# Kernel optimization log

Measured on AMD Instinct MI355X. Metric: run time of the kernel, lower is better.

The kernel has to match this reference:

```python
import jax, jax.numpy as jnp
import numpy as np

DIM = 768
HEADS = 12
HEAD_DIM = DIM // HEADS
ROPE_BASE = 100.0  # Dust3R uses freq=100 for its rotary embedding


def apply_rope(x):
    # x: [B, H, N, D] -> rotary embedding over token index (rotate-half form)
    B, H, N, D = x.shape
    pos = jnp.arange(N, dtype=jnp.float32)
    inv_freq = 1.0 / (ROPE_BASE ** (jnp.arange(0, D, 2, dtype=jnp.float32) / D))
    ang = pos[:, None] * inv_freq[None, :]            # [N, D/2]
    cos = jnp.concatenate([jnp.cos(ang), jnp.cos(ang)], axis=-1).astype(x.dtype)  # [N, D]
    sin = jnp.concatenate([jnp.sin(ang), jnp.sin(ang)], axis=-1).astype(x.dtype)
    x1, x2 = jnp.split(x, 2, axis=-1)
    x_rot = jnp.concatenate([-x2, x1], axis=-1)
    return x * cos + x_rot * sin


def setup_inputs() -> dict:
    key = jax.random.key(0)
    ks = jax.random.split(key, 8)
    B, N = 8, 1024
    scale = 0.02
    return {
        "query": jax.random.normal(ks[0], (B, N, DIM), jnp.float32),
        "key": jax.random.normal(ks[1], (B, N, DIM), jnp.float32),
        "value": jax.random.normal(ks[2], (B, N, DIM), jnp.float32),
        "Wq": jax.random.normal(ks[3], (DIM, DIM), jnp.float32) * scale,
        "Wk": jax.random.normal(ks[4], (DIM, DIM), jnp.float32) * scale,
        "Wv": jax.random.normal(ks[5], (DIM, DIM), jnp.float32) * scale,
        "Wo": jax.random.normal(ks[6], (DIM, DIM), jnp.float32) * scale,
        "bo": jax.random.normal(ks[7], (DIM,), jnp.float32) * scale,
    }


def reference(query, key, value, Wq, Wk, Wv, Wo, bo):
    B, Nq, C = query.shape
    H, D = HEADS, HEAD_DIM
    sm_scale = D ** -0.5
    # Linear projections (torch Linear: x @ W.T), split heads -> [B, H, N, D]
    q = jnp.einsum('bnc,dc->bnd', query, Wq).reshape(B, Nq, H, D).transpose(0, 2, 1, 3)
    k = jnp.einsum('bnc,dc->bnd', key, Wk).reshape(B, -1, H, D).transpose(0, 2, 1, 3)
    v = jnp.einsum('bnc,dc->bnd', value, Wv).reshape(B, -1, H, D).transpose(0, 2, 1, 3)
    q = apply_rope(q)
    k = apply_rope(k)
    attn = jnp.einsum('bhqd,bhkd->bhqk', q, k) * sm_scale
    attn = jax.nn.softmax(attn, axis=-1)
    x = jnp.einsum('bhqk,bhkd->bhqd', attn, v)
    x = x.transpose(0, 2, 1, 3).reshape(B, Nq, C)
    return jnp.einsum('bnc,dc->bnd', x, Wo) + bo
```

## Files before the change

### kernel.cpp

```cpp
#include <hip/hip_runtime.h>
#include <cmath>

typedef __bf16 bf16x8 __attribute__((ext_vector_type(8)));
typedef float f32x4 __attribute__((ext_vector_type(4)));
typedef unsigned short u16;

#define MFMA_BF16 __builtin_amdgcn_mfma_f32_16x16x32_bf16

__device__ __forceinline__ u16 f2bf(float f) {
  unsigned int u = __float_as_uint(f);
  u = (u + 0x7fffu + ((u >> 16) & 1u)) >> 16;
  return (u16)u;
}

__device__ __forceinline__ void async16(const u16* g, u16* l) {
  __builtin_amdgcn_global_load_lds(
      (__attribute__((address_space(1))) void*)g,
      (__attribute__((address_space(3))) void*)l, 16, 0, 0);
}

__global__ __launch_bounds__(256) void cvt_bf16(const float4* __restrict__ in,
                                                uint2* __restrict__ out, int n4) {
  int i = blockIdx.x * 256 + threadIdx.x;
  if (i >= n4) return;
  float4 f = in[i];
  uint2 o;
  o.x = (unsigned)f2bf(f.x) | ((unsigned)f2bf(f.y) << 16);
  o.y = (unsigned)f2bf(f.z) | ((unsigned)f2bf(f.w) << 16);
  out[i] = o;
}

__global__ __launch_bounds__(256) void cvt_all(
    const float4* s0, const float4* s1, const float4* s2, const float4* s3,
    const float4* s4, const float4* s5, const float4* s6,
    uint2* d0, uint2* d1, uint2* d2, uint2* d3, uint2* d4, uint2* d5, uint2* d6) {
  int i = blockIdx.x * 256 + threadIdx.x;
  const float4* src;
  uint2* dst;
  int off;
  if (i < 1572864)      { src = s0; dst = d0; off = i; }
  else if (i < 3145728) { src = s1; dst = d1; off = i - 1572864; }
  else if (i < 4718592) { src = s2; dst = d2; off = i - 3145728; }
  else {
    int j = i - 4718592;
    int w = j / 147456;
    off = j - w * 147456;
    src = (w == 0) ? s3 : (w == 1) ? s4 : (w == 2) ? s5 : s6;
    dst = (w == 0) ? d3 : (w == 1) ? d4 : (w == 2) ? d5 : d6;
  }
  float4 f = src[off];
  uint2 o;
  o.x = (unsigned)f2bf(f.x) | ((unsigned)f2bf(f.y) << 16);
  o.y = (unsigned)f2bf(f.z) | ((unsigned)f2bf(f.w) << 16);
  dst[off] = o;
}

__device__ __forceinline__ void gemm_body(const u16* __restrict__ Ag,
                                          const u16* __restrict__ Wg,
                                          void* __restrict__ OutP,
                                          const float* __restrict__ bias,
                                          int mode, int bx, int by) {
  __shared__ u16 As[128][64];
  __shared__ u16 Bs[64][64];
  const int tid  = threadIdx.x;
  const int lane = tid & 63, wv = tid >> 6;
  const int l15  = lane & 15, quad = lane >> 4;
  const int row0 = bx * 128, col0 = by * 64;
  const int wm = wv * 32;
  const int swA = l15 & 7;

  f32x4 acc[2][4];
#pragma unroll
  for (int i = 0; i < 2; ++i)
#pragma unroll
    for (int j = 0; j < 4; ++j) acc[i][j] = (f32x4){0.f, 0.f, 0.f, 0.f};

  for (int kb0 = 0; kb0 < 768; kb0 += 64) {
#pragma unroll
    for (int rr = 0; rr < 4; ++rr) {
      int c = rr * 256 + tid;
      int row = c >> 3, cp = c & 7;
      int gc = cp ^ (row & 7);
      async16(&Ag[(size_t)(row0 + row) * 768 + kb0 + gc * 8], &As[row][cp * 8]);
    }
#pragma unroll
    for (int rr = 0; rr < 2; ++rr) {
      int c = rr * 256 + tid;
      int row = c >> 3, cp = c & 7;
      int gc = cp ^ (row & 7);
      async16(&Wg[(size_t)(col0 + row) * 768 + kb0 + gc * 8], &Bs[row][cp * 8]);
    }
    __syncthreads();
#pragma unroll
    for (int kd = 0; kd < 2; ++kd) {
      int cpk = (((kd * 4 + quad) ^ swA)) * 8;
      bf16x8 af[2], bfr[4];
      af[0] = *(const bf16x8*)&As[wm + l15][cpk];
      af[1] = *(const bf16x8*)&As[wm + 16 + l15][cpk];
#pragma unroll
      for (int nt = 0; nt < 4; ++nt) bfr[nt] = *(const bf16x8*)&Bs[nt * 16 + l15][cpk];
#pragma unroll
      for (int mt = 0; mt < 2; ++mt)
#pragma unroll
        for (int nt = 0; nt < 4; ++nt)
          acc[mt][nt] = MFMA_BF16(af[mt], bfr[nt], acc[mt][nt], 0, 0, 0);
    }
    __syncthreads();
  }

  if (mode == 3) {
    float* O = (float*)OutP;
#pragma unroll
    for (int mt = 0; mt < 2; ++mt)
#pragma unroll
      for (int r = 0; r < 4; ++r) {
        int m = row0 + wm + mt * 16 + quad * 4 + r;
#pragma unroll
        for (int nt = 0; nt < 4; ++nt) {
          int c = col0 + nt * 16 + l15;
          O[(size_t)m * 768 + c] = acc[mt][nt][r] + bias[c];
        }
      }
  } else if (mode == 2) {
    u16* O = (u16*)OutP;
#pragma unroll
    for (int mt = 0; mt < 2; ++mt)
#pragma unroll
      for (int r = 0; r < 4; ++r) {
        int m = row0 + wm + mt * 16 + quad * 4 + r;
        int b = m >> 10, n = m & 1023;
#pragma unroll
        for (int nt = 0; nt < 4; ++nt) {
          int c = col0 + nt * 16 + l15;
          O[(size_t)(b * 768 + c) * 1024 + n] = f2bf(acc[mt][nt][r]);
        }
      }
  } else {
    u16* O = (u16*)OutP;
    const float scale = (mode == 0) ? 0.125f * 1.44269504088896f : 1.0f;
    const float invf0 = exp2f(-6.6438561897747395f * (float)l15 * (1.0f / 32.0f));
    const float invf1 = exp2f(-6.6438561897747395f * (float)(16 + l15) * (1.0f / 32.0f));
#pragma unroll
    for (int mt = 0; mt < 2; ++mt)
#pragma unroll
      for (int r = 0; r < 4; ++r) {
        int m = row0 + wm + mt * 16 + quad * 4 + r;
        int b = m >> 10, n = m & 1023;
        float fn = (float)n;
        size_t rowbase = (size_t)b * 786432 + (size_t)n * 64;
#pragma unroll
        for (int nt = 0; nt < 2; ++nt) {
          float sv, cv;
          __sincosf(fn * (nt ? invf1 : invf0), &sv, &cv);
          float x1 = acc[mt][nt][r], x2 = acc[mt][nt + 2][r];
          int c1 = col0 + nt * 16 + l15;
          int c2 = c1 + 32;
          O[rowbase + (size_t)(c1 >> 6) * 65536 + (c1 & 63)] = f2bf((x1 * cv - x2 * sv) * scale);
          O[rowbase + (size_t)(c2 >> 6) * 65536 + (c2 & 63)] = f2bf((x2 * cv + x1 * sv) * scale);
        }
      }
  }
}

__global__ __launch_bounds__(256, 3) void gemm768(const u16* __restrict__ A,
                                                  const u16* __restrict__ W,
                                                  void* __restrict__ OutP,
                                                  const float* __restrict__ bias,
                                                  int mode) {
  gemm_body(A, W, OutP, bias, mode, blockIdx.x, blockIdx.y);
}

__global__ __launch_bounds__(256, 3) void gemm_qkv(
    const u16* __restrict__ xq, const u16* __restrict__ xk, const u16* __restrict__ xv,
    const u16* __restrict__ wq, const u16* __restrict__ wk, const u16* __restrict__ wv,
    u16* __restrict__ qb, u16* __restrict__ kb, u16* __restrict__ vtb) {
  int z = blockIdx.z;
  const u16* A = (z == 0) ? xq : (z == 1) ? xk : xv;
  const u16* W = (z == 0) ? wq : (z == 1) ? wk : wv;
  void* O      = (z == 0) ? (void*)qb : (z == 1) ? (void*)kb : (void*)vtb;
  gemm_body(A, W, O, nullptr, z, blockIdx.x, blockIdx.y);
}

__global__ __launch_bounds__(256, 2) void attn_fused(const u16* __restrict__ Q,
                                                     const u16* __restrict__ K,
                                                     const u16* __restrict__ Vt,
                                                     u16* __restrict__ X) {
  __shared__ u16 KsF[2 * 64 * 32];
  __shared__ u16 VsF[2 * 64 * 32];
  __shared__ u16 Ps[128 * 88];

  const int tid  = threadIdx.x;
  const int lane = tid & 63, wv = tid >> 6;
  const int l15  = lane & 15, quad = lane >> 4;
  const int bh = blockIdx.x, qt = blockIdx.y;
  const size_t base = (size_t)bh * 65536;
  const int sw8 = (quad ^ ((l15 >> 1) & 3)) * 8;

  const u16* Qg = Q + base + (size_t)qt * 8192;
#pragma unroll
  for (int rr = 0; rr < 4; ++rr) {
    int c = rr * 256 + tid;
    async16(&Qg[c * 8], &Ps[c * 8]);
  }
  __syncthreads();
  bf16x8 qf[2][2];
#pragma unroll
  for (int mt = 0; mt < 2; ++mt)
#pragma unroll
    for (int kd = 0; kd < 2; ++kd)
      qf[mt][kd] = *(const bf16x8*)&Ps[(wv * 32 + mt * 16 + l15) * 64 + kd * 32 + quad * 8];
  __syncthreads();

  f32x4 o[2][4];
  float lsum[2][4];
#pragma unroll
  for (int mt = 0; mt < 2; ++mt) {
#pragma unroll
    for (int nt = 0; nt < 4; ++nt) o[mt][nt] = (f32x4){0.f, 0.f, 0.f, 0.f};
#pragma unroll
    for (int r = 0; r < 4; ++r) lsum[mt][r] = 0.f;
  }

  const u16* Kb = K + base;
  const u16* Vb = Vt + base;

  for (int kt = 0; kt < 1024; kt += 64) {
#pragma unroll
    for (int rr = 0; rr < 2; ++rr) {
      int c = rr * 256 + tid;
      int sub = c >> 8, rowi = (c >> 2) & 63, colc = c & 3;
      int cs = (colc ^ ((rowi >> 1) & 3)) * 8;
      async16(&Kb[(size_t)(kt + rowi) * 64 + sub * 32 + cs], &KsF[c * 8]);
      async16(&Vb[(size_t)rowi * 1024 + kt + sub * 32 + cs], &VsF[c * 8]);
    }
    __syncthreads();

    f32x4 s[2][4];
#pragma unroll
    for (int ct = 0; ct < 4; ++ct) {
      bf16x8 kf0 = *(const bf16x8*)&KsF[(ct * 16 + l15) * 32 + sw8];
      bf16x8 kf1 = *(const bf16x8*)&KsF[2048 + (ct * 16 + l15) * 32 + sw8];
#pragma unroll
      for (int mt = 0; mt < 2; ++mt) {
        f32x4 t = (f32x4){0.f, 0.f, 0.f, 0.f};
        t = MFMA_BF16(qf[mt][0], kf0, t, 0, 0, 0);
        t = MFMA_BF16(qf[mt][1], kf1, t, 0, 0, 0);
        s[mt][ct] = t;
      }
    }

#pragma unroll
    for (int mt = 0; mt < 2; ++mt)
#pragma unroll
      for (int ct = 0; ct < 4; ++ct)
#pragma unroll
        for (int r = 0; r < 4; ++r) {
          float p = __builtin_amdgcn_exp2f(s[mt][ct][r]);
          lsum[mt][r] += p;
          unsigned u = __float_as_uint(p);
          Ps[(wv * 32 + mt * 16 + quad * 4 + r) * 88 + ct * 16 + l15] =
              (u16)((u + 0x8000u) >> 16);
        }

#pragma unroll
    for (int ks = 0; ks < 2; ++ks) {
      bf16x8 pf0 = *(const bf16x8*)&Ps[(wv * 32 + l15) * 88 + ks * 32 + quad * 8];
      bf16x8 pf1 = *(const bf16x8*)&Ps[(wv * 32 + 16 + l15) * 88 + ks * 32 + quad * 8];
#pragma unroll
      for (int nt = 0; nt < 4; ++nt) {
        bf16x8 vf = *(const bf16x8*)&VsF[ks * 2048 + (nt * 16 + l15) * 32 + sw8];
        o[0][nt] = MFMA_BF16(pf0, vf, o[0][nt], 0, 0, 0);
        o[1][nt] = MFMA_BF16(pf1, vf, o[1][nt], 0, 0, 0);
      }
    }
    __syncthreads();
  }

  const int b = bh / 12, h = bh % 12;
#pragma unroll
  for (int mt = 0; mt < 2; ++mt)
#pragma unroll
    for (int r = 0; r < 4; ++r) {
      float l = lsum[mt][r];
#pragma unroll
      for (int d = 1; d < 16; d <<= 1) l += __shfl_xor(l, d, 16);
      float inv = __builtin_amdgcn_rcpf(l);
      int n = qt * 128 + wv * 32 + mt * 16 + quad * 4 + r;
      size_t rowoff = ((size_t)(b * 1024 + n)) * 768 + h * 64;
#pragma unroll
      for (int nt = 0; nt < 4; ++nt)
        X[rowoff + nt * 16 + l15] = f2bf(o[mt][nt][r] * inv);
    }
}

extern "C" void kernel_launch(void* const* d_in, const int* in_sizes, int n_in,
                              void* d_out, int out_size, void* d_ws, size_t ws_size,
                              hipStream_t stream) {
  const float* qin = (const float*)d_in[0];
  const float* kin = (const float*)d_in[1];
  const float* vin = (const float*)d_in[2];
  const float* Wq  = (const float*)d_in[3];
  const float* Wk  = (const float*)d_in[4];
  const float* Wv  = (const float*)d_in[5];
  const float* Wo  = (const float*)d_in[6];
  const float* bo  = (const float*)d_in[7];
  char* ws = (char*)d_ws;

  if (ws_size >= 80216064) {
    u16* xq16 = (u16*)(ws + 0);
    u16* xk16 = (u16*)(ws + 12582912);
    u16* xv16 = (u16*)(ws + 25165824);
    u16* qb   = (u16*)(ws + 37748736);
    u16* kb   = (u16*)(ws + 50331648);
    u16* vtb  = (u16*)(ws + 62914560);
    u16* wq16 = (u16*)(ws + 75497472);
    u16* wk16 = wq16 + 589824;
    u16* wv16 = wk16 + 589824;
    u16* wo16 = wv16 + 589824;
    u16* X    = xq16;

    cvt_all<<<20736, 256, 0, stream>>>(
        (const float4*)qin, (const float4*)kin, (const float4*)vin,
        (const float4*)Wq, (const float4*)Wk, (const float4*)Wv, (const float4*)Wo,
        (uint2*)xq16, (uint2*)xk16, (uint2*)xv16,
        (uint2*)wq16, (uint2*)wk16, (uint2*)wv16, (uint2*)wo16);
    gemm_qkv<<<dim3(64, 12, 3), 256, 0, stream>>>(xq16, xk16, xv16, wq16, wk16, wv16,
                                                  qb, kb, vtb);
    attn_fused<<<dim3(96, 8), 256, 0, stream>>>(qb, kb, vtb, X);
    gemm768<<<dim3(64, 12), 256, 0, stream>>>(X, wo16, d_out, bo, 3);
  } else {
    u16* xbuf = (u16*)(ws + 0);
    u16* qb   = (u16*)(ws + 12582912);
    u16* kb   = (u16*)(ws + 25165824);
    u16* vtb  = (u16*)(ws + 37748736);
    u16* wq16 = (u16*)(ws + 50331648);
    u16* wk16 = wq16 + 589824;
    u16* wv16 = wk16 + 589824;
    u16* wo16 = wv16 + 589824;

    cvt_bf16<<<576, 256, 0, stream>>>((const float4*)Wq, (uint2*)wq16, 147456);
    cvt_bf16<<<576, 256, 0, stream>>>((const float4*)Wk, (uint2*)wk16, 147456);
    cvt_bf16<<<576, 256, 0, stream>>>((const float4*)Wv, (uint2*)wv16, 147456);
    cvt_bf16<<<576, 256, 0, stream>>>((const float4*)Wo, (uint2*)wo16, 147456);

    dim3 ggrid(64, 12);
    cvt_bf16<<<6144, 256, 0, stream>>>((const float4*)qin, (uint2*)xbuf, 1572864);
    gemm768<<<ggrid, 256, 0, stream>>>(xbuf, wq16, (void*)qb, nullptr, 0);
    cvt_bf16<<<6144, 256, 0, stream>>>((const float4*)kin, (uint2*)xbuf, 1572864);
    gemm768<<<ggrid, 256, 0, stream>>>(xbuf, wk16, (void*)kb, nullptr, 1);
    cvt_bf16<<<6144, 256, 0, stream>>>((const float4*)vin, (uint2*)xbuf, 1572864);
    gemm768<<<ggrid, 256, 0, stream>>>(xbuf, wv16, (void*)vtb, nullptr, 2);

    attn_fused<<<dim3(96, 8), 256, 0, stream>>>(qb, kb, vtb, xbuf);

    gemm768<<<ggrid, 256, 0, stream>>>(xbuf, wo16, d_out, bo, 3);
  }
}
```

Baseline: 214.5 us.

## Widen QKV GEMM tiles to 128x128 and process 128 keys per attention stage

The QKV projection now uses a dedicated kernel with 128x128 output tiles, where each wave computes a 64x64 sub-tile. This raises operand reuse per LDS load and halves the number of blocks. The attention kernel loads 128 keys/values per barrier and processes them as two 64-key halves, halving the number of syncs. It also shrinks the P buffer padding and raises its occupancy hint to 3, and the output GEMM's hint goes to 4. The changes trade more registers and LDS per block for fewer barriers and fewer global reloads, at the risk of spilling or lower occupancy.

After: 235.3 us. +9.7%, slower.

```diff
diff --git a/kernel.cpp b/kernel.cpp
--- a/kernel.cpp
+++ b/kernel.cpp
@@ -55,6 +55,65 @@
   dst[off] = o;
 }
 
+template <int MT>
+__device__ __forceinline__ void gemm_epilogue(f32x4 (&acc)[MT][4], void* OutP,
+                                              const float* bias, int mode,
+                                              int row0, int colbase, int wm,
+                                              int l15, int quad) {
+  if (mode == 3) {
+    float* O = (float*)OutP;
+#pragma unroll
+    for (int mt = 0; mt < MT; ++mt)
+#pragma unroll
+      for (int r = 0; r < 4; ++r) {
+        int m = row0 + wm + mt * 16 + quad * 4 + r;
+#pragma unroll
+        for (int nt = 0; nt < 4; ++nt) {
+          int c = colbase + nt * 16 + l15;
+          O[(size_t)m * 768 + c] = acc[mt][nt][r] + bias[c];
+        }
+      }
+  } else if (mode == 2) {
+    u16* O = (u16*)OutP;
+#pragma unroll
+    for (int mt = 0; mt < MT; ++mt)
+#pragma unroll
+      for (int r = 0; r < 4; ++r) {
+        int m = row0 + wm + mt * 16 + quad * 4 + r;
+        int b = m >> 10, n = m & 1023;
+#pragma unroll
+        for (int nt = 0; nt < 4; ++nt) {
+          int c = colbase + nt * 16 + l15;
+          O[(size_t)(b * 768 + c) * 1024 + n] = f2bf(acc[mt][nt][r]);
+        }
+      }
+  } else {
+    u16* O = (u16*)OutP;
+    const float scale = (mode == 0) ? 0.125f * 1.44269504088896f : 1.0f;
+    const float invf0 = exp2f(-6.6438561897747395f * (float)l15 * (1.0f / 32.0f));
+    const float invf1 = exp2f(-6.6438561897747395f * (float)(16 + l15) * (1.0f / 32.0f));
+#pragma unroll
+    for (int mt = 0; mt < MT; ++mt)
+#pragma unroll
+      for (int r = 0; r < 4; ++r) {
+        int m = row0 + wm + mt * 16 + quad * 4 + r;
+        int b = m >> 10, n = m & 1023;
+        float fn = (float)n;
+        size_t rowbase = (size_t)b * 786432 + (size_t)n * 64;
+#pragma unroll
+        for (int nt = 0; nt < 2; ++nt) {
+          float sv, cv;
+          __sincosf(fn * (nt ? invf1 : invf0), &sv, &cv);
+          float x1 = acc[mt][nt][r], x2 = acc[mt][nt + 2][r];
+          int c1 = colbase + nt * 16 + l15;
+          int c2 = c1 + 32;
+          O[rowbase + (size_t)(c1 >> 6) * 65536 + (c1 & 63)] = f2bf((x1 * cv - x2 * sv) * scale);
+          O[rowbase + (size_t)(c2 >> 6) * 65536 + (c2 & 63)] = f2bf((x2 * cv + x1 * sv) * scale);
+        }
+      }
+  }
+}
+
 __device__ __forceinline__ void gemm_body(const u16* __restrict__ Ag,
                                           const u16* __restrict__ Wg,
                                           void* __restrict__ OutP,
@@ -63,10 +122,10 @@
   __shared__ u16 As[128][64];
   __shared__ u16 Bs[64][64];
   const int tid  = threadIdx.x;
-  const int lane = tid & 63, wv = tid >> 6;
+  const int lane = tid & 63, wvid = tid >> 6;
   const int l15  = lane & 15, quad = lane >> 4;
   const int row0 = bx * 128, col0 = by * 64;
-  const int wm = wv * 32;
+  const int wm = wvid * 32;
   const int swA = l15 & 7;
 
   f32x4 acc[2][4];
@@ -107,62 +166,10 @@
     }
     __syncthreads();
   }
-
-  if (mode == 3) {
-    float* O = (float*)OutP;
-#pragma unroll
-    for (int mt = 0; mt < 2; ++mt)
-#pragma unroll
-      for (int r = 0; r < 4; ++r) {
-        int m = row0 + wm + mt * 16 + quad * 4 + r;
-#pragma unroll
-        for (int nt = 0; nt < 4; ++nt) {
-          int c = col0 + nt * 16 + l15;
-          O[(size_t)m * 768 + c] = acc[mt][nt][r] + bias[c];
-        }
-      }
-  } else if (mode == 2) {
-    u16* O = (u16*)OutP;
-#pragma unroll
-    for (int mt = 0; mt < 2; ++mt)
-#pragma unroll
-      for (int r = 0; r < 4; ++r) {
-        int m = row0 + wm + mt * 16 + quad * 4 + r;
-        int b = m >> 10, n = m & 1023;
-#pragma unroll
-        for (int nt = 0; nt < 4; ++nt) {
-          int c = col0 + nt * 16 + l15;
-          O[(size_t)(b * 768 + c) * 1024 + n] = f2bf(acc[mt][nt][r]);
-        }
-      }
-  } else {
-    u16* O = (u16*)OutP;
-    const float scale = (mode == 0) ? 0.125f * 1.44269504088896f : 1.0f;
-    const float invf0 = exp2f(-6.6438561897747395f * (float)l15 * (1.0f / 32.0f));
-    const float invf1 = exp2f(-6.6438561897747395f * (float)(16 + l15) * (1.0f / 32.0f));
-#pragma unroll
-    for (int mt = 0; mt < 2; ++mt)
-#pragma unroll
-      for (int r = 0; r < 4; ++r) {
-        int m = row0 + wm + mt * 16 + quad * 4 + r;
-        int b = m >> 10, n = m & 1023;
-        float fn = (float)n;
-        size_t rowbase = (size_t)b * 786432 + (size_t)n * 64;
-#pragma unroll
-        for (int nt = 0; nt < 2; ++nt) {
-          float sv, cv;
-          __sincosf(fn * (nt ? invf1 : invf0), &sv, &cv);
-          float x1 = acc[mt][nt][r], x2 = acc[mt][nt + 2][r];
-          int c1 = col0 + nt * 16 + l15;
-          int c2 = c1 + 32;
-          O[rowbase + (size_t)(c1 >> 6) * 65536 + (c1 & 63)] = f2bf((x1 * cv - x2 * sv) * scale);
-          O[rowbase + (size_t)(c2 >> 6) * 65536 + (c2 & 63)] = f2bf((x2 * cv + x1 * sv) * scale);
-        }
-      }
-  }
-}
-
-__global__ __launch_bounds__(256, 3) void gemm768(const u16* __restrict__ A,
+  gemm_epilogue<2>(acc, OutP, bias, mode, row0, col0, wm, l15, quad);
+}
+
+__global__ __launch_bounds__(256, 4) void gemm768(const u16* __restrict__ A,
                                                   const u16* __restrict__ W,
                                                   void* __restrict__ OutP,
                                                   const float* __restrict__ bias,
@@ -170,27 +177,76 @@
   gemm_body(A, W, OutP, bias, mode, blockIdx.x, blockIdx.y);
 }
 
-__global__ __launch_bounds__(256, 3) void gemm_qkv(
+__global__ __launch_bounds__(256, 3) void gemm_qkv_wide(
     const u16* __restrict__ xq, const u16* __restrict__ xk, const u16* __restrict__ xv,
-    const u16* __restrict__ wq, const u16* __restrict__ wk, const u16* __restrict__ wv,
+    const u16* __restrict__ wgq, const u16* __restrict__ wgk, const u16* __restrict__ wgv,
     u16* __restrict__ qb, u16* __restrict__ kb, u16* __restrict__ vtb) {
-  int z = blockIdx.z;
-  const u16* A = (z == 0) ? xq : (z == 1) ? xk : xv;
-  const u16* W = (z == 0) ? wq : (z == 1) ? wk : wv;
-  void* O      = (z == 0) ? (void*)qb : (z == 1) ? (void*)kb : (void*)vtb;
-  gemm_body(A, W, O, nullptr, z, blockIdx.x, blockIdx.y);
-}
-
-__global__ __launch_bounds__(256, 2) void attn_fused(const u16* __restrict__ Q,
+  const int mode = blockIdx.z;
+  const u16* Ag = (mode == 0) ? xq : (mode == 1) ? xk : xv;
+  const u16* Wg = (mode == 0) ? wgq : (mode == 1) ? wgk : wgv;
+  void* OutP    = (mode == 0) ? (void*)qb : (mode == 1) ? (void*)kb : (void*)vtb;
+
+  __shared__ u16 As[128][64];
+  __shared__ u16 Bs[128][64];
+  const int tid  = threadIdx.x;
+  const int lane = tid & 63, wvid = tid >> 6;
+  const int l15  = lane & 15, quad = lane >> 4;
+  const int row0 = blockIdx.x * 128, col0 = blockIdx.y * 128;
+  const int wm = (wvid >> 1) * 64, wn = (wvid & 1) * 64;
+  const int swA = l15 & 7;
+
+  f32x4 acc[4][4];
+#pragma unroll
+  for (int i = 0; i < 4; ++i)
+#pragma unroll
+    for (int j = 0; j < 4; ++j) acc[i][j] = (f32x4){0.f, 0.f, 0.f, 0.f};
+
+  for (int kb0 = 0; kb0 < 768; kb0 += 64) {
+#pragma unroll
+    for (int rr = 0; rr < 4; ++rr) {
+      int c = rr * 256 + tid;
+      int row = c >> 3, cp = c & 7;
+      int gc = cp ^ (row & 7);
+      async16(&Ag[(size_t)(row0 + row) * 768 + kb0 + gc * 8], &As[row][cp * 8]);
+    }
+#pragma unroll
+    for (int rr = 0; rr < 4; ++rr) {
+      int c = rr * 256 + tid;
+      int row = c >> 3, cp = c & 7;
+      int gc = cp ^ (row & 7);
+      async16(&Wg[(size_t)(col0 + row) * 768 + kb0 + gc * 8], &Bs[row][cp * 8]);
+    }
+    __syncthreads();
+#pragma unroll
+    for (int kd = 0; kd < 2; ++kd) {
+      int cpk = (((kd * 4 + quad) ^ swA)) * 8;
+      bf16x8 af[4], bfr[4];
+#pragma unroll
+      for (int t = 0; t < 4; ++t) {
+        af[t]  = *(const bf16x8*)&As[wm + t * 16 + l15][cpk];
+        bfr[t] = *(const bf16x8*)&Bs[wn + t * 16 + l15][cpk];
+      }
+#pragma unroll
+      for (int mt = 0; mt < 4; ++mt)
+#pragma unroll
+        for (int nt = 0; nt < 4; ++nt)
+          acc[mt][nt] = MFMA_BF16(af[mt], bfr[nt], acc[mt][nt], 0, 0, 0);
+    }
+    __syncthreads();
+  }
+  gemm_epilogue<4>(acc, OutP, nullptr, mode, row0, col0 + wn, wm, l15, quad);
+}
+
+__global__ __launch_bounds__(256, 3) void attn_fused(const u16* __restrict__ Q,
                                                      const u16* __restrict__ K,
                                                      const u16* __restrict__ Vt,
                                                      u16* __restrict__ X) {
-  __shared__ u16 KsF[2 * 64 * 32];
-  __shared__ u16 VsF[2 * 64 * 32];
-  __shared__ u16 Ps[128 * 88];
+  __shared__ u16 KsF[8192];
+  __shared__ u16 VsF[8192];
+  __shared__ u16 Ps[128 * 72];
 
   const int tid  = threadIdx.x;
-  const int lane = tid & 63, wv = tid >> 6;
+  const int lane = tid & 63, wvid = tid >> 6;
   const int l15  = lane & 15, quad = lane >> 4;
   const int bh = blockIdx.x, qt = blockIdx.y;
   const size_t base = (size_t)bh * 65536;
@@ -208,7 +264,7 @@
   for (int mt = 0; mt < 2; ++mt)
 #pragma unroll
     for (int kd = 0; kd < 2; ++kd)
-      qf[mt][kd] = *(const bf16x8*)&Ps[(wv * 32 + mt * 16 + l15) * 64 + kd * 32 + quad * 8];
+      qf[mt][kd] = *(const bf16x8*)&Ps[(wvid * 32 + mt * 16 + l15) * 64 + kd * 32 + quad * 8];
   __syncthreads();
 
   f32x4 o[2][4];
@@ -224,53 +280,60 @@
   const u16* Kb = K + base;
   const u16* Vb = Vt + base;
 
-  for (int kt = 0; kt < 1024; kt += 64) {
-#pragma unroll
-    for (int rr = 0; rr < 2; ++rr) {
+  for (int kt = 0; kt < 1024; kt += 128) {
+#pragma unroll
+    for (int rr = 0; rr < 4; ++rr) {
       int c = rr * 256 + tid;
-      int sub = c >> 8, rowi = (c >> 2) & 63, colc = c & 3;
+      int half = c >> 9, rem = c & 511;
+      int sub = rem >> 8, rowi = (rem >> 2) & 63, colc = rem & 3;
       int cs = (colc ^ ((rowi >> 1) & 3)) * 8;
-      async16(&Kb[(size_t)(kt + rowi) * 64 + sub * 32 + cs], &KsF[c * 8]);
-      async16(&Vb[(size_t)rowi * 1024 + kt + sub * 32 + cs], &VsF[c * 8]);
-    }
-    __syncthreads();
-
-    f32x4 s[2][4];
-#pragma unroll
-    for (int ct = 0; ct < 4; ++ct) {
-      bf16x8 kf0 = *(const bf16x8*)&KsF[(ct * 16 + l15) * 32 + sw8];
-      bf16x8 kf1 = *(const bf16x8*)&KsF[2048 + (ct * 16 + l15) * 32 + sw8];
-#pragma unroll
-      for (int mt = 0; mt < 2; ++mt) {
-        f32x4 t = (f32x4){0.f, 0.f, 0.f, 0.f};
-        t = MFMA_BF16(qf[mt][0], kf0, t, 0, 0, 0);
-        t = MFMA_BF16(qf[mt][1], kf1, t, 0, 0, 0);
-        s[mt][ct] = t;
-      }
-    }
-
-#pragma unroll
-    for (int mt = 0; mt < 2; ++mt)
-#pragma unroll
-      for (int ct = 0; ct < 4; ++ct)
-#pragma unroll
-        for (int r = 0; r < 4; ++r) {
-          float p = __builtin_amdgcn_exp2f(s[mt][ct][r]);
-          lsum[mt][r] += p;
-          unsigned u = __float_as_uint(p);
-          Ps[(wv * 32 + mt * 16 + quad * 4 + r) * 88 + ct * 16 + l15] =
-              (u16)((u + 0x8000u) >> 16);
+      async16(&Kb[(size_t)(kt + half * 64 + rowi) * 64 + sub * 32 + cs], &KsF[c * 8]);
+      async16(&Vb[(size_t)rowi * 1024 + kt + half * 64 + sub * 32 + cs], &VsF[c * 8]);
+    }
+    __syncthreads();
+
+#pragma unroll
+    for (int hf = 0; hf < 2; ++hf) {
+      const u16* Kh = KsF + hf * 4096;
+      const u16* Vh = VsF + hf * 4096;
+
+      f32x4 s[2][4];
+#pragma unroll
+      for (int ct = 0; ct < 4; ++ct) {
+        bf16x8 kf0 = *(const bf16x8*)&Kh[(ct * 16 + l15) * 32 + sw8];
+        bf16x8 kf1 = *(const bf16x8*)&Kh[2048 + (ct * 16 + l15) * 32 + sw8];
+#pragma unroll
+        for (int mt = 0; mt < 2; ++mt) {
+          f32x4 t = (f32x4){0.f, 0.f, 0.f, 0.f};
+          t = MFMA_BF16(qf[mt][0], kf0, t, 0, 0, 0);
+          t = MFMA_BF16(qf[mt][1], kf1, t, 0, 0, 0);
+          s[mt][ct] = t;
         }
-
-#pragma unroll
-    for (int ks = 0; ks < 2; ++ks) {
-      bf16x8 pf0 = *(const bf16x8*)&Ps[(wv * 32 + l15) * 88 + ks * 32 + quad * 8];
-      bf16x8 pf1 = *(const bf16x8*)&Ps[(wv * 32 + 16 + l15) * 88 + ks * 32 + quad * 8];
-#pragma unroll
-      for (int nt = 0; nt < 4; ++nt) {
-        bf16x8 vf = *(const bf16x8*)&VsF[ks * 2048 + (nt * 16 + l15) * 32 + sw8];
-        o[0][nt] = MFMA_BF16(pf0, vf, o[0][nt], 0, 0, 0);
-        o[1][nt] = MFMA_BF16(pf1, vf, o[1][nt], 0, 0, 0);
+      }
+
+#pragma unroll
+      for (int mt = 0; mt < 2; ++mt)
+#pragma unroll
+        for (int ct = 0; ct < 4; ++ct)
+#pragma unroll
+          for (int r = 0; r < 4; ++r) {
+            float p = __builtin_amdgcn_exp2f(s[mt][ct][r]);
+            lsum[mt][r] += p;
+            unsigned u = __float_as_uint(p);
+            Ps[(wvid * 32 + mt * 16 + quad * 4 + r) * 72 + ct * 16 + l15] =
+                (u16)((u + 0x8000u) >> 16);
+          }
+
+#pragma unroll
+      for (int ks = 0; ks < 2; ++ks) {
+        bf16x8 pf0 = *(const bf16x8*)&Ps[(wvid * 32 + l15) * 72 + ks * 32 + quad * 8];
+        bf16x8 pf1 = *(const bf16x8*)&Ps[(wvid * 32 + 16 + l15) * 72 + ks * 32 + quad * 8];
+#pragma unroll
+        for (int nt = 0; nt < 4; ++nt) {
+          bf16x8 vf = *(const bf16x8*)&Vh[ks * 2048 + (nt * 16 + l15) * 32 + sw8];
+          o[0][nt] = MFMA_BF16(pf0, vf, o[0][nt], 0, 0, 0);
+          o[1][nt] = MFMA_BF16(pf1, vf, o[1][nt], 0, 0, 0);
+        }
       }
     }
     __syncthreads();
@@ -285,7 +348,7 @@
 #pragma unroll
       for (int d = 1; d < 16; d <<= 1) l += __shfl_xor(l, d, 16);
       float inv = __builtin_amdgcn_rcpf(l);
-      int n = qt * 128 + wv * 32 + mt * 16 + quad * 4 + r;
+      int n = qt * 128 + wvid * 32 + mt * 16 + quad * 4 + r;
       size_t rowoff = ((size_t)(b * 1024 + n)) * 768 + h * 64;
 #pragma unroll
       for (int nt = 0; nt < 4; ++nt)
@@ -324,8 +387,9 @@
         (const float4*)Wq, (const float4*)Wk, (const float4*)Wv, (const float4*)Wo,
         (uint2*)xq16, (uint2*)xk16, (uint2*)xv16,
         (uint2*)wq16, (uint2*)wk16, (uint2*)wv16, (uint2*)wo16);
-    gemm_qkv<<<dim3(64, 12, 3), 256, 0, stream>>>(xq16, xk16, xv16, wq16, wk16, wv16,
-                                                  qb, kb, vtb);
+    gemm_qkv_wide<<<dim3(64, 6, 3), 256, 0, stream>>>(xq16, xk16, xv16,
+                                                      wq16, wk16, wv16,
+                                                      qb, kb, vtb);
     attn_fused<<<dim3(96, 8), 256, 0, stream>>>(qb, kb, vtb, X);
     gemm768<<<dim3(64, 12), 256, 0, stream>>>(X, wo16, d_out, bo, 3);
   } else {
```
